# Kernel optimization log

Hardware: AMD Instinct MI355X
Metric: run time of the kernel (lower is better)

## Reference

```python
import jax, jax.numpy as jnp
import numpy as np

CROP_H = 14
CROP_W = 14
EXTRAPOLATION_VALUE = 0.0


def _crop_and_resize(image, boxes, box_ind, crop_h, crop_w, extrapolation_value):
    # image: [B, C, H, W], boxes: [N, 4] normalized (y1, x1, y2, x2), box_ind: [N]
    B, C, H, W = image.shape
    y1, x1, y2, x2 = boxes[:, 0], boxes[:, 1], boxes[:, 2], boxes[:, 3]

    # TF crop_and_resize coordinate mapping (crop_h, crop_w > 1 case)
    height_scale = (y2 - y1) * (H - 1) / (crop_h - 1)  # [N]
    width_scale = (x2 - x1) * (W - 1) / (crop_w - 1)   # [N]
    iy = jnp.arange(crop_h, dtype=image.dtype)
    ix = jnp.arange(crop_w, dtype=image.dtype)
    in_y = y1[:, None] * (H - 1) + iy[None, :] * height_scale[:, None]  # [N, crop_h]
    in_x = x1[:, None] * (W - 1) + ix[None, :] * width_scale[:, None]   # [N, crop_w]

    valid_y = (in_y >= 0) & (in_y <= H - 1)  # [N, crop_h]
    valid_x = (in_x >= 0) & (in_x <= W - 1)  # [N, crop_w]

    top = jnp.floor(in_y)
    left = jnp.floor(in_x)
    ly = (in_y - top)[:, :, None, None]   # [N, crop_h, 1, 1]
    lx = (in_x - left)[:, None, :, None]  # [N, 1, crop_w, 1]

    top_i = jnp.clip(top.astype(jnp.int32), 0, H - 1)          # [N, crop_h]
    bot_i = jnp.clip(top_i + 1, 0, H - 1)
    left_i = jnp.clip(left.astype(jnp.int32), 0, W - 1)        # [N, crop_w]
    right_i = jnp.clip(left_i + 1, 0, W - 1)

    b = box_ind[:, None, None]            # [N, 1, 1]
    yt = top_i[:, :, None]                # [N, crop_h, 1]
    yb = bot_i[:, :, None]
    xl = left_i[:, None, :]               # [N, 1, crop_w]
    xr = right_i[:, None, :]

    # advanced indexing -> [N, crop_h, crop_w, C]
    tl = image[b, :, yt, xl]
    tr = image[b, :, yt, xr]
    bl = image[b, :, yb, xl]
    br = image[b, :, yb, xr]

    top_v = tl + (tr - tl) * lx
    bot_v = bl + (br - bl) * lx
    val = top_v + (bot_v - top_v) * ly    # [N, crop_h, crop_w, C]

    mask = (valid_y[:, :, None] & valid_x[:, None, :])[:, :, :, None]
    val = jnp.where(mask, val, jnp.asarray(extrapolation_value, image.dtype))
    return jnp.transpose(val, (0, 3, 1, 2))  # [N, C, crop_h, crop_w]


def setup_inputs() -> dict:
    key = jax.random.key(0)
    k1, k2, k3 = jax.random.split(key, 3)
    B, C, H, W = 8, 256, 200, 200
    N = 1000
    image = jax.random.normal(k1, (B, C, H, W), dtype=jnp.float32)
    boxes = jax.random.uniform(k2, (N, 4), dtype=jnp.float32)
    box_ind = jax.random.randint(k3, (N,), 0, B, dtype=jnp.int32)
    return {"image": image, "boxes": boxes, "box_ind": box_ind}


def reference(image, boxes, box_ind):
    return _crop_and_resize(image, boxes, box_ind, CROP_H, CROP_W, EXTRAPOLATION_VALUE)
```

## Files before the change

### kernel.cpp

```cpp
#include <hip/hip_runtime.h>


#define CROP_H 14
#define CROP_W 14
#define C_DIM 256
#define H_DIM 200
#define W_DIM 200
#define HW (H_DIM * W_DIM)
#define PER_BOX (C_DIM * CROP_H * CROP_W)
#define BLOCK 256
#define CHUNKS 4
#define C_PER (C_DIM / CHUNKS)
#define ELEMS (C_PER * CROP_H * CROP_W)

__global__ __launch_bounds__(BLOCK) void sort_boxes_kernel(
    const int* __restrict__ box_ind, int N, int* __restrict__ perm)
{
    __shared__ int cnt[8];
    __shared__ int base[8];
    const int t = threadIdx.x;
    if (t < 8) cnt[t] = 0;
    __syncthreads();
    for (int i = t; i < N; i += BLOCK) atomicAdd(&cnt[box_ind[i]], 1);
    __syncthreads();
    if (t == 0) {
        int run = 0;
        for (int b = 0; b < 8; ++b) { base[b] = run; run += cnt[b]; }
    }
    __syncthreads();
    for (int i = t; i < N; i += BLOCK) {
        const int pos = atomicAdd(&base[box_ind[i]], 1);
        perm[pos] = i;
    }
}

__global__ __launch_bounds__(BLOCK) void crop_and_resize_kernel(
    const float* __restrict__ image,
    const float* __restrict__ boxes,
    const int*   __restrict__ box_ind,
    const int*   __restrict__ perm,
    float*       __restrict__ out)
{
    __shared__ int   s_ti[CROP_H], s_bi[CROP_H];
    __shared__ int   s_li[CROP_W], s_ri[CROP_W];
    __shared__ float s_ly[CROP_H], s_lx[CROP_W];
    __shared__ int   s_vy[CROP_H], s_vx[CROP_W];
    __shared__ int   s_b;

    const int slot  = blockIdx.x / CHUNKS;
    const int chunk = blockIdx.x % CHUNKS;
    const int t     = threadIdx.x;

    __shared__ int s_n;
    if (t == 0) s_n = perm[slot];
    __syncthreads();
    const int n = s_n;

    if (t == 0) s_b = box_ind[n];
    if (t < CROP_H + CROP_W) {
        const float y1 = boxes[n * 4 + 0];
        const float x1 = boxes[n * 4 + 1];
        const float y2 = boxes[n * 4 + 2];
        const float x2 = boxes[n * 4 + 3];
        if (t < CROP_H) {
            const int iy = t;
            const float hs   = (y2 - y1) * (float)(H_DIM - 1) / (float)(CROP_H - 1);
            const float in_y = y1 * (float)(H_DIM - 1) + (float)iy * hs;
            const int   vy   = (in_y >= 0.0f) && (in_y <= (float)(H_DIM - 1));
            const float top  = floorf(in_y);
            const float ly   = in_y - top;
            int ti = (int)top;
            ti = min(max(ti, 0), H_DIM - 1);
            const int bi = min(ti + 1, H_DIM - 1);
            s_ti[iy] = ti; s_bi[iy] = bi; s_ly[iy] = ly; s_vy[iy] = vy;
        } else {
            const int ix = t - CROP_H;
            const float ws   = (x2 - x1) * (float)(W_DIM - 1) / (float)(CROP_W - 1);
            const float in_x = x1 * (float)(W_DIM - 1) + (float)ix * ws;
            const int   vx   = (in_x >= 0.0f) && (in_x <= (float)(W_DIM - 1));
            const float left = floorf(in_x);
            const float lx   = in_x - left;
            int li = (int)left;
            li = min(max(li, 0), W_DIM - 1);
            const int ri = min(li + 1, W_DIM - 1);
            s_li[ix] = li; s_ri[ix] = ri; s_lx[ix] = lx; s_vx[ix] = vx;
        }
    }
    __syncthreads();

    const float* __restrict__ imgb = image + (size_t)s_b * (C_DIM * HW)
                                           + (size_t)chunk * (C_PER * HW);
    float* __restrict__ outb = out + (size_t)n * PER_BOX + (size_t)chunk * ELEMS;

    #pragma unroll 4
    for (int j = t; j < ELEMS; j += BLOCK) {
        const int c  = j / (CROP_H * CROP_W);
        const int p  = j - c * (CROP_H * CROP_W);
        const int iy = p / CROP_W;
        const int ix = p - iy * CROP_W;

        const int ti = s_ti[iy], bi = s_bi[iy];
        const int li = s_li[ix], ri = s_ri[ix];
        const float* __restrict__ base = imgb + (size_t)c * HW;

        const float tl = base[ti * W_DIM + li];
        const float tr = base[ti * W_DIM + ri];
        const float bl = base[bi * W_DIM + li];
        const float br = base[bi * W_DIM + ri];

        const float lx = s_lx[ix];
        const float ly = s_ly[iy];
        const float top_v = tl + (tr - tl) * lx;
        const float bot_v = bl + (br - bl) * lx;
        float v = top_v + (bot_v - top_v) * ly;

        v = (s_vy[iy] & s_vx[ix]) ? v : 0.0f;
        outb[j] = v;
    }
}

extern "C" void kernel_launch(void* const* d_in, const int* in_sizes, int n_in,
                              void* d_out, int out_size, void* d_ws, size_t ws_size,
                              hipStream_t stream) {
    const float* image   = (const float*)d_in[0];
    const float* boxes   = (const float*)d_in[1];
    const int*   box_ind = (const int*)d_in[2];
    float*       out     = (float*)d_out;
    int*         perm    = (int*)d_ws;

    const int N = in_sizes[2];

    sort_boxes_kernel<<<dim3(1), dim3(BLOCK), 0, stream>>>(box_ind, N, perm);
    crop_and_resize_kernel<<<dim3(N * CHUNKS), dim3(BLOCK), 0, stream>>>(
        image, boxes, box_ind, perm, out);
}
```

Before: 704.3 us.

## Remap workgroups across XCDs and precompute per-pixel gather offsets in LDS

Reorders the grid so that consecutive workgroups landing on the same XCD handle adjacent sorted boxes within one channel chunk, improving L2 locality of image reads. Each of the 196 crop pixels gets a precomputed base offset, right/bottom deltas, validity flag and weights stored in LDS, so the inner loop does fewer shared loads and less index arithmetic. The loop gets a fixed trip count with unroll 7, uses fma, and launch bounds now request 6 blocks per CU. The remap relies on the grid being divisible by 8 and on an assumed round-robin workgroup-to-XCD dispatch.

```diff
diff --git a/kernel.cpp b/kernel.cpp
--- a/kernel.cpp
+++ b/kernel.cpp
@@ -3,15 +3,18 @@
 
 #define CROP_H 14
 #define CROP_W 14
+#define CROP_HW (CROP_H * CROP_W)
 #define C_DIM 256
 #define H_DIM 200
 #define W_DIM 200
 #define HW (H_DIM * W_DIM)
-#define PER_BOX (C_DIM * CROP_H * CROP_W)
+#define PER_BOX (C_DIM * CROP_HW)
 #define BLOCK 256
 #define CHUNKS 4
 #define C_PER (C_DIM / CHUNKS)
-#define ELEMS (C_PER * CROP_H * CROP_W)
+#define ELEMS (C_PER * CROP_HW)
+#define ITERS (ELEMS / BLOCK)
+#define NXCD 8
 
 __global__ __launch_bounds__(BLOCK) void sort_boxes_kernel(
     const int* __restrict__ box_ind, int N, int* __restrict__ perm)
@@ -34,57 +37,66 @@
     }
 }
 
-__global__ __launch_bounds__(BLOCK) void crop_and_resize_kernel(
+__global__ __launch_bounds__(BLOCK, 6) void crop_and_resize_kernel(
     const float* __restrict__ image,
     const float* __restrict__ boxes,
     const int*   __restrict__ box_ind,
     const int*   __restrict__ perm,
-    float*       __restrict__ out)
+    float*       __restrict__ out,
+    int N)
 {
-    __shared__ int   s_ti[CROP_H], s_bi[CROP_H];
-    __shared__ int   s_li[CROP_W], s_ri[CROP_W];
-    __shared__ float s_ly[CROP_H], s_lx[CROP_W];
-    __shared__ int   s_vy[CROP_H], s_vx[CROP_W];
-    __shared__ int   s_b;
+    __shared__ int4   s_d[CROP_HW];
+    __shared__ float2 s_w[CROP_HW];
+    __shared__ int s_n, s_b;
 
-    const int slot  = blockIdx.x / CHUNKS;
-    const int chunk = blockIdx.x % CHUNKS;
+    const int nwg = gridDim.x;
+    int wgid = blockIdx.x;
+    if ((nwg % NXCD) == 0) {
+        const int per = nwg / NXCD;
+        wgid = (wgid % NXCD) * per + wgid / NXCD;
+    }
+    const int chunk = wgid / N;
+    const int slot  = wgid - chunk * N;
     const int t     = threadIdx.x;
 
-    __shared__ int s_n;
-    if (t == 0) s_n = perm[slot];
+    if (t == 0) {
+        const int n = perm[slot];
+        s_n = n;
+        s_b = box_ind[n];
+    }
     __syncthreads();
     const int n = s_n;
 
-    if (t == 0) s_b = box_ind[n];
-    if (t < CROP_H + CROP_W) {
+    if (t < CROP_HW) {
+        const int iy = t / CROP_W;
+        const int ix = t - iy * CROP_W;
         const float y1 = boxes[n * 4 + 0];
         const float x1 = boxes[n * 4 + 1];
         const float y2 = boxes[n * 4 + 2];
         const float x2 = boxes[n * 4 + 3];
-        if (t < CROP_H) {
-            const int iy = t;
-            const float hs   = (y2 - y1) * (float)(H_DIM - 1) / (float)(CROP_H - 1);
-            const float in_y = y1 * (float)(H_DIM - 1) + (float)iy * hs;
-            const int   vy   = (in_y >= 0.0f) && (in_y <= (float)(H_DIM - 1));
-            const float top  = floorf(in_y);
-            const float ly   = in_y - top;
-            int ti = (int)top;
-            ti = min(max(ti, 0), H_DIM - 1);
-            const int bi = min(ti + 1, H_DIM - 1);
-            s_ti[iy] = ti; s_bi[iy] = bi; s_ly[iy] = ly; s_vy[iy] = vy;
-        } else {
-            const int ix = t - CROP_H;
-            const float ws   = (x2 - x1) * (float)(W_DIM - 1) / (float)(CROP_W - 1);
-            const float in_x = x1 * (float)(W_DIM - 1) + (float)ix * ws;
-            const int   vx   = (in_x >= 0.0f) && (in_x <= (float)(W_DIM - 1));
-            const float left = floorf(in_x);
-            const float lx   = in_x - left;
-            int li = (int)left;
-            li = min(max(li, 0), W_DIM - 1);
-            const int ri = min(li + 1, W_DIM - 1);
-            s_li[ix] = li; s_ri[ix] = ri; s_lx[ix] = lx; s_vx[ix] = vx;
-        }
+
+        const float hs   = (y2 - y1) * (float)(H_DIM - 1) / (float)(CROP_H - 1);
+        const float ws   = (x2 - x1) * (float)(W_DIM - 1) / (float)(CROP_W - 1);
+        const float in_y = y1 * (float)(H_DIM - 1) + (float)iy * hs;
+        const float in_x = x1 * (float)(W_DIM - 1) + (float)ix * ws;
+
+        const int vy = (in_y >= 0.0f) && (in_y <= (float)(H_DIM - 1));
+        const int vx = (in_x >= 0.0f) && (in_x <= (float)(W_DIM - 1));
+
+        const float top  = floorf(in_y);
+        const float left = floorf(in_x);
+        const float ly   = in_y - top;
+        const float lx   = in_x - left;
+
+        int ti = (int)top;
+        ti = min(max(ti, 0), H_DIM - 1);
+        const int bi = min(ti + 1, H_DIM - 1);
+        int li = (int)left;
+        li = min(max(li, 0), W_DIM - 1);
+        const int ri = min(li + 1, W_DIM - 1);
+
+        s_d[t] = make_int4(ti * W_DIM + li, ri - li, (bi - ti) * W_DIM, vy & vx);
+        s_w[t] = make_float2(ly, lx);
     }
     __syncthreads();
 
@@ -92,29 +104,25 @@
                                            + (size_t)chunk * (C_PER * HW);
     float* __restrict__ outb = out + (size_t)n * PER_BOX + (size_t)chunk * ELEMS;
 
-    #pragma unroll 4
-    for (int j = t; j < ELEMS; j += BLOCK) {
-        const int c  = j / (CROP_H * CROP_W);
-        const int p  = j - c * (CROP_H * CROP_W);
-        const int iy = p / CROP_W;
-        const int ix = p - iy * CROP_W;
+    #pragma unroll 7
+    for (int k = 0; k < ITERS; ++k) {
+        const int j = t + k * BLOCK;
+        const int c = j / CROP_HW;
+        const int p = j - c * CROP_HW;
 
-        const int ti = s_ti[iy], bi = s_bi[iy];
-        const int li = s_li[ix], ri = s_ri[ix];
-        const float* __restrict__ base = imgb + (size_t)c * HW;
+        const int4   d = s_d[p];
+        const float2 w = s_w[p];
 
-        const float tl = base[ti * W_DIM + li];
-        const float tr = base[ti * W_DIM + ri];
-        const float bl = base[bi * W_DIM + li];
-        const float br = base[bi * W_DIM + ri];
+        const float* __restrict__ basec = imgb + (size_t)c * HW + d.x;
+        const float tl = basec[0];
+        const float tr = basec[d.y];
+        const float bl = basec[d.z];
+        const float br = basec[d.z + d.y];
 
-        const float lx = s_lx[ix];
-        const float ly = s_ly[iy];
-        const float top_v = tl + (tr - tl) * lx;
-        const float bot_v = bl + (br - bl) * lx;
-        float v = top_v + (bot_v - top_v) * ly;
-
-        v = (s_vy[iy] & s_vx[ix]) ? v : 0.0f;
+        const float top_v = fmaf(tr - tl, w.y, tl);
+        const float bot_v = fmaf(br - bl, w.y, bl);
+        float v = fmaf(bot_v - top_v, w.x, top_v);
+        v = d.w ? v : 0.0f;
         outb[j] = v;
     }
 }
@@ -132,5 +140,5 @@
 
     sort_boxes_kernel<<<dim3(1), dim3(BLOCK), 0, stream>>>(box_ind, N, perm);
     crop_and_resize_kernel<<<dim3(N * CHUNKS), dim3(BLOCK), 0, stream>>>(
-        image, boxes, box_ind, perm, out);
+        image, boxes, box_ind, perm, out, N);
 }
```

After: 708.3 us. Within noise of the previous version (+0.6%).
